# Performance work log

Hardware: AMD Instinct MI355X
Metric: run time of the kernel (lower is better)

The kernel has to match this reference:

```python
import jax, jax.numpy as jnp
import numpy as np

# (dy, dx) offsets corresponding to the single -1 entries of kernels 1..8
# delta1 rows: (0,0),(0,1),(0,2),(1,2); delta2 = spatial flip: (2,2),(2,1),(2,0),(1,0)
OFFSETS = [(-1, -1), (-1, 0), (-1, 1), (0, 1), (1, 1), (1, 0), (1, -1), (0, -1)]
NUM_LAYER = 9
EPS = 1e-12


def _shift(x, dy, dx):
    # zero-padded shift: out[y, x] = in[y + dy, x + dx]; dilation = shifts[0] = 1
    b, c, h, w = x.shape
    p = jnp.pad(x, ((0, 0), (0, 0), (1, 1), (1, 1)))
    return jax.lax.dynamic_slice(p, (0, 0, 1 + dy, 1 + dx), (b, c, h, w))


def _l2norm(v, axis):
    # matches torch.nn.functional.normalize: v / max(||v||, eps)
    n = jnp.sqrt(jnp.sum(v * v, axis=axis, keepdims=True))
    return v / jnp.maximum(n, EPS)


def setup_inputs() -> dict:
    key = jax.random.key(0)
    k1, k2, k3, k4 = jax.random.split(key, 4)
    B, C, H, W = 4, 256, 96, 96
    cen = jax.random.normal(k1, (B, C, H, W), dtype=jnp.float32)
    scale = 1.0 / np.sqrt(C)
    # grouped 1x1 convs (groups=9): per-group (C x C) weight matrices
    W1 = jax.random.normal(k2, (NUM_LAYER, C, C), dtype=jnp.float32) * scale
    W2 = jax.random.normal(k3, (C, C), dtype=jnp.float32) * scale
    W3 = jax.random.normal(k4, (NUM_LAYER, C, C), dtype=jnp.float32) * scale
    return {"cen": cen, "W1": W1, "W2": W2, "W3": W3}


def reference(cen, W1, W2, W3):
    b, c, h, w = cen.shape
    # Extract_layer: 8 fixed depthwise 3x3 convs (each = negated shift) + identity
    surrounds = jnp.stack(
        [-_shift(cen, dy, dx) for dy, dx in OFFSETS] + [cen], axis=1
    )  # (b, 9, c, h, w)
    # Analyze_layer: grouped 1x1 convs = per-group matmuls
    out1 = jnp.einsum("gij,bgjhw->bgihw", W1, surrounds)
    out2 = jnp.einsum("ij,bjhw->bihw", W2, cen)[:, None]  # (b, 1, c, h, w)
    out3 = jnp.einsum("gij,bgjhw->bgihw", W3, surrounds)
    out1 = _l2norm(out1, axis=2)
    out2 = _l2norm(out2, axis=2)
    out3 = _l2norm(out3, axis=2)
    # softmax over a size-1 axis (dim=2 after mean+keepdim) -> identically 1.0
    att = jax.nn.softmax(
        jnp.mean(out1 * out2, axis=2, keepdims=True), axis=2
    )  # (b, 9, 1, h, w)
    out = jnp.sum(att * out3, axis=1)  # (b, c, h, w)
    return out + cen
```

## Files before the change

kernel.cpp:

```cpp
#include <hip/hip_runtime.h>
#include <stdint.h>

#define BB 4
#define CC 256
#define HH 96
#define WW 96
#define HP 98
#define CP 264
#define XT 32
#define YT 4
#define XE 34

typedef __bf16 bf16x8 __attribute__((ext_vector_type(8)));
typedef __bf16 bf16x16 __attribute__((ext_vector_type(16)));
typedef float f32x4 __attribute__((ext_vector_type(4)));
typedef float f32x16 __attribute__((ext_vector_type(16)));

__device__ __forceinline__ uint16_t f2bf(float f) {
    uint32_t u = __float_as_uint(f);
    u += 0x7FFFu + ((u >> 16) & 1u);
    return (uint16_t)(u >> 16);
}

__global__ void zero_halo(uint16_t* __restrict__ cenT) {
    int idx = blockIdx.x * 256 + threadIdx.x;
    if (idx >= 1552 * 33) return;
    int p = idx / 33, q = idx - p * 33;
    int b = p / 388, s = p - b * 388;
    int y, x;
    if (s < 98)      { y = 0;       x = s; }
    else if (s < 196){ y = 97;      x = s - 98; }
    else if (s < 292){ x = 0;       y = s - 196 + 1; }
    else             { x = 97;      y = s - 292 + 1; }
    size_t o = (((size_t)b * HP + y) * HP + x) * CP + q * 8;
    *(uint4*)(cenT + o) = make_uint4(0u, 0u, 0u, 0u);
}

__global__ void transpose_cen(const float* __restrict__ cen, uint16_t* __restrict__ cenT) {
    const int y = blockIdx.x, b = blockIdx.y, ch = blockIdx.z, tid = threadIdx.x;
    __shared__ uint16_t ldsX[128 * 100];

    #pragma unroll
    for (int i = 0; i < 12; ++i) {
        int f = i * 256 + tid;
        int c = f / 24, xq = f % 24;
        float4 v = *(const float4*)(cen + ((((size_t)b * CC + ch * 128 + c) * HH + y) * WW + xq * 4));
        uint2 pk;
        pk.x = (uint32_t)f2bf(v.x) | ((uint32_t)f2bf(v.y) << 16);
        pk.y = (uint32_t)f2bf(v.z) | ((uint32_t)f2bf(v.w) << 16);
        *(uint2*)(&ldsX[c * 100 + xq * 4]) = pk;
    }
    __syncthreads();
    #pragma unroll
    for (int i = 0; i < 6; ++i) {
        int t = i * 256 + tid;
        int x = t % 96, cq = t / 96;
        uint32_t w0, w1, w2, w3;
        w0 = (uint32_t)ldsX[(cq * 8 + 0) * 100 + x] | ((uint32_t)ldsX[(cq * 8 + 1) * 100 + x] << 16);
        w1 = (uint32_t)ldsX[(cq * 8 + 2) * 100 + x] | ((uint32_t)ldsX[(cq * 8 + 3) * 100 + x] << 16);
        w2 = (uint32_t)ldsX[(cq * 8 + 4) * 100 + x] | ((uint32_t)ldsX[(cq * 8 + 5) * 100 + x] << 16);
        w3 = (uint32_t)ldsX[(cq * 8 + 6) * 100 + x] | ((uint32_t)ldsX[(cq * 8 + 7) * 100 + x] << 16);
        size_t o = (((size_t)b * HP + (y + 1)) * HP + (x + 1)) * CP + ch * 128 + cq * 8;
        *(uint4*)(cenT + o) = make_uint4(w0, w1, w2, w3);
    }
}

__global__ void cvt_w3(const float* __restrict__ W3, uint16_t* __restrict__ W3bf) {
    int e = (blockIdx.x * 256 + threadIdx.x) * 4;
    int g = e >> 16, n = (e >> 8) & 255, k = e & 255;
    float4 v = *(const float4*)(W3 + e);
    uint2 pk;
    pk.x = (uint32_t)f2bf(v.x) | ((uint32_t)f2bf(v.y) << 16);
    pk.y = (uint32_t)f2bf(v.z) | ((uint32_t)f2bf(v.w) << 16);
    size_t o = (size_t)(((g * 8 + (n >> 5)) * 16 + (k >> 4)) * 512)
             + (n & 31) * 16 + ((k >> 3) & 1) * 8 + (k & 7);
    *(uint2*)(W3bf + o) = pk;
}

__global__ __launch_bounds__(512, 2)
void ecm_main(const float* __restrict__ cen, const uint16_t* __restrict__ cenT,
              const uint16_t* __restrict__ W3bf, float* __restrict__ out) {
    const int tid = threadIdx.x;
    const int wv = tid >> 6, lane = tid & 63, col = lane & 31, kh = lane >> 5;
    const int c2 = wv & 3, p2 = wv >> 2;
    const int x0 = blockIdx.x * XT, y0 = blockIdx.y * YT, b = blockIdx.z;

    __shared__ __align__(16) uint16_t ldsA[6 * XE * CP];
    __shared__ __align__(16) float ldsP[2][128][4];

    const int dgOrd[9] = {0, 1, 2, 7, 8, 3, 6, 5, 4};

    for (int rr = 0; rr < 6; ++rr) {
        const uint4* gs = (const uint4*)(cenT + (((size_t)b * HP + (y0 + rr)) * HP + x0) * CP);
        uint4* ls = (uint4*)(ldsA + rr * XE * CP);
        for (int c = tid; c < XE * CP / 8; c += 512) ls[c] = gs[c];
    }
    __syncthreads();

    const uint16_t* wbA = W3bf + (size_t)(2 * c2) * (16 * 512) + col * 16 + kh * 8;
    bf16x16 finA0 = {}, finA1 = {}, finB0 = {}, finB1 = {};

    #pragma unroll 1
    for (int idx = 0; idx < 9; ++idx) {
        const int g = dgOrd[idx], dg = idx / 3, dx = idx % 3 - 1;

        const uint16_t* wgA = wbA + (size_t)g * 65536;
        const uint16_t* wgB = wgA + 16 * 512;
        const int a0 = ((dg + 2 * p2) * XE + (col + dx + 1)) * CP + kh * 8;
        const int a1 = a0 + XE * CP;

        f32x16 aA0 = {}, aA1 = {}, aB0 = {}, aB1 = {};

        bf16x8 qA[3], qB[3];
        #pragma unroll
        for (int i = 0; i < 3; ++i) {
            qA[i] = *(const bf16x8*)(wgA + i * 512);
            qB[i] = *(const bf16x8*)(wgB + i * 512);
        }
        bf16x8 b0 = *(const bf16x8*)(ldsA + a0);
        bf16x8 b1 = *(const bf16x8*)(ldsA + a1);

        #pragma unroll
        for (int ks = 0; ks < 16; ++ks) {
            bf16x8 wa = qA[ks % 3], wb = qB[ks % 3];
            if (ks + 3 < 16) {
                qA[ks % 3] = *(const bf16x8*)(wgA + (ks + 3) * 512);
                qB[ks % 3] = *(const bf16x8*)(wgB + (ks + 3) * 512);
            }
            bf16x8 n0 = b0, n1 = b1;
            if (ks + 1 < 16) {
                n0 = *(const bf16x8*)(ldsA + a0 + (ks + 1) * 16);
                n1 = *(const bf16x8*)(ldsA + a1 + (ks + 1) * 16);
            }
            __builtin_amdgcn_s_setprio(1);
            aA0 = __builtin_amdgcn_mfma_f32_32x32x16_bf16(wa, b0, aA0, 0, 0, 0);
            aB0 = __builtin_amdgcn_mfma_f32_32x32x16_bf16(wb, b0, aB0, 0, 0, 0);
            aA1 = __builtin_amdgcn_mfma_f32_32x32x16_bf16(wa, b1, aA1, 0, 0, 0);
            aB1 = __builtin_amdgcn_mfma_f32_32x32x16_bf16(wb, b1, aB1, 0, 0, 0);
            __builtin_amdgcn_s_setprio(0);
            b0 = n0; b1 = n1;
        }

        float s0 = 0.f, s1 = 0.f;
        #pragma unroll
        for (int r = 0; r < 16; ++r) {
            s0 += aA0[r] * aA0[r] + aB0[r] * aB0[r];
            s1 += aA1[r] * aA1[r] + aB1[r] * aB1[r];
        }
        s0 += __shfl_xor(s0, 32, 64);
        s1 += __shfl_xor(s1, 32, 64);
        if (kh == 0) {
            ldsP[idx & 1][(2 * p2) * 32 + col][c2] = s0;
            ldsP[idx & 1][(2 * p2 + 1) * 32 + col][c2] = s1;
        }
        __syncthreads();

        f32x4 pa = *(const f32x4*)&ldsP[idx & 1][(2 * p2) * 32 + col][0];
        f32x4 qa = *(const f32x4*)&ldsP[idx & 1][(2 * p2 + 1) * 32 + col][0];
        float n0 = pa[0] + pa[1] + pa[2] + pa[3];
        float n1 = qa[0] + qa[1] + qa[2] + qa[3];
        const float sgn = (g == 8) ? 1.f : -1.f;
        float sc0 = sgn / fmaxf(sqrtf(n0), 1e-12f);
        float sc1 = sgn / fmaxf(sqrtf(n1), 1e-12f);
        #pragma unroll
        for (int r = 0; r < 16; ++r) {
            finA0[r] = (__bf16)((float)finA0[r] + aA0[r] * sc0);
            finB0[r] = (__bf16)((float)finB0[r] + aB0[r] * sc0);
            finA1[r] = (__bf16)((float)finA1[r] + aA1[r] * sc1);
            finB1[r] = (__bf16)((float)finB1[r] + aB1[r] * sc1);
        }
    }

    #pragma unroll
    for (int r = 0; r < 16; ++r) {
        int chA = c2 * 64 + (r & 3) + 8 * (r >> 2) + 4 * kh;
        size_t oA0 = (((size_t)b * CC + chA) * HH + (y0 + 2 * p2)) * WW + (x0 + col);
        size_t oA1 = oA0 + WW;
        out[oA0] = (float)finA0[r] + cen[oA0];
        out[oA1] = (float)finA1[r] + cen[oA1];
        size_t oB0 = oA0 + (size_t)32 * HH * WW;
        size_t oB1 = oB0 + WW;
        out[oB0] = (float)finB0[r] + cen[oB0];
        out[oB1] = (float)finB1[r] + cen[oB1];
    }
}

extern "C" void kernel_launch(void* const* d_in, const int* in_sizes, int n_in,
                              void* d_out, int out_size, void* d_ws, size_t ws_size,
                              hipStream_t stream) {
    const float* cen = (const float*)d_in[0];
    const float* W3 = (const float*)d_in[3];
    float* out = (float*)d_out;

    uint16_t* cenT = (uint16_t*)d_ws;
    const size_t cenT_elems = (size_t)BB * HP * HP * CP;
    uint16_t* W3bf = cenT + cenT_elems;

    zero_halo<<<201, 256, 0, stream>>>(cenT);
    transpose_cen<<<dim3(HH, BB, 2), 256, 0, stream>>>(cen, cenT);
    cvt_w3<<<576, 256, 0, stream>>>(W3, W3bf);
    ecm_main<<<dim3(3, 24, 4), 512, 0, stream>>>(cen, cenT, W3bf, out);
}
```

Measured before the change: 185.6 us.

## Enlarge spatial tile to six rows so each wave computes three rows

Raises the tile height from 4 to 6 rows so each wave accumulates three output rows per weight fragment instead of two. This reuses each loaded W3 fragment across more MFMAs and lowers the relative halo load. In exchange it uses much more LDS, more accumulator registers and fewer blocks, and weight prefetch depth drops from three to two. That can reduce occupancy and leave compute units idle.

```diff
diff --git a/kernel.cpp b/kernel.cpp
--- a/kernel.cpp
+++ b/kernel.cpp
@@ -8,7 +8,7 @@
 #define HP 98
 #define CP 264
 #define XT 32
-#define YT 4
+#define YT 6
 #define XE 34
 
 typedef __bf16 bf16x8 __attribute__((ext_vector_type(8)));
@@ -82,15 +82,15 @@
               const uint16_t* __restrict__ W3bf, float* __restrict__ out) {
     const int tid = threadIdx.x;
     const int wv = tid >> 6, lane = tid & 63, col = lane & 31, kh = lane >> 5;
-    const int c2 = wv & 3, p2 = wv >> 2;
+    const int c2 = wv & 3, p3 = wv >> 2;
     const int x0 = blockIdx.x * XT, y0 = blockIdx.y * YT, b = blockIdx.z;
 
-    __shared__ __align__(16) uint16_t ldsA[6 * XE * CP];
-    __shared__ __align__(16) float ldsP[2][128][4];
+    __shared__ __align__(16) uint16_t ldsA[8 * XE * CP];
+    __shared__ __align__(16) float ldsP[2][192][4];
 
     const int dgOrd[9] = {0, 1, 2, 7, 8, 3, 6, 5, 4};
 
-    for (int rr = 0; rr < 6; ++rr) {
+    for (int rr = 0; rr < 8; ++rr) {
         const uint4* gs = (const uint4*)(cenT + (((size_t)b * HP + (y0 + rr)) * HP + x0) * CP);
         uint4* ls = (uint4*)(ldsA + rr * XE * CP);
         for (int c = tid; c < XE * CP / 8; c += 512) ls[c] = gs[c];
@@ -98,7 +98,7 @@
     __syncthreads();
 
     const uint16_t* wbA = W3bf + (size_t)(2 * c2) * (16 * 512) + col * 16 + kh * 8;
-    bf16x16 finA0 = {}, finA1 = {}, finB0 = {}, finB1 = {};
+    bf16x16 fA[3] = {}, fB[3] = {};
 
     #pragma unroll 1
     for (int idx = 0; idx < 9; ++idx) {
@@ -106,82 +106,85 @@
 
         const uint16_t* wgA = wbA + (size_t)g * 65536;
         const uint16_t* wgB = wgA + 16 * 512;
-        const int a0 = ((dg + 2 * p2) * XE + (col + dx + 1)) * CP + kh * 8;
-        const int a1 = a0 + XE * CP;
-
-        f32x16 aA0 = {}, aA1 = {}, aB0 = {}, aB1 = {};
-
-        bf16x8 qA[3], qB[3];
-        #pragma unroll
-        for (int i = 0; i < 3; ++i) {
-            qA[i] = *(const bf16x8*)(wgA + i * 512);
-            qB[i] = *(const bf16x8*)(wgB + i * 512);
-        }
-        bf16x8 b0 = *(const bf16x8*)(ldsA + a0);
-        bf16x8 b1 = *(const bf16x8*)(ldsA + a1);
+        int a[3];
+        #pragma unroll
+        for (int rr = 0; rr < 3; ++rr)
+            a[rr] = ((dg + 3 * p3 + rr) * XE + (col + dx + 1)) * CP + kh * 8;
+
+        f32x16 aA[3] = {}, aB[3] = {};
+
+        bf16x8 qA[2], qB[2];
+        qA[0] = *(const bf16x8*)(wgA);
+        qB[0] = *(const bf16x8*)(wgB);
+        qA[1] = *(const bf16x8*)(wgA + 512);
+        qB[1] = *(const bf16x8*)(wgB + 512);
+        bf16x8 bR[3];
+        #pragma unroll
+        for (int rr = 0; rr < 3; ++rr) bR[rr] = *(const bf16x8*)(ldsA + a[rr]);
 
         #pragma unroll
         for (int ks = 0; ks < 16; ++ks) {
-            bf16x8 wa = qA[ks % 3], wb = qB[ks % 3];
-            if (ks + 3 < 16) {
-                qA[ks % 3] = *(const bf16x8*)(wgA + (ks + 3) * 512);
-                qB[ks % 3] = *(const bf16x8*)(wgB + (ks + 3) * 512);
+            bf16x8 wa = qA[ks & 1], wb = qB[ks & 1];
+            if (ks + 2 < 16) {
+                qA[ks & 1] = *(const bf16x8*)(wgA + (ks + 2) * 512);
+                qB[ks & 1] = *(const bf16x8*)(wgB + (ks + 2) * 512);
             }
-            bf16x8 n0 = b0, n1 = b1;
-            if (ks + 1 < 16) {
-                n0 = *(const bf16x8*)(ldsA + a0 + (ks + 1) * 16);
-                n1 = *(const bf16x8*)(ldsA + a1 + (ks + 1) * 16);
+            bf16x8 bN[3];
+            #pragma unroll
+            for (int rr = 0; rr < 3; ++rr)
+                bN[rr] = (ks + 1 < 16) ? *(const bf16x8*)(ldsA + a[rr] + (ks + 1) * 16)
+                                       : bR[rr];
+            __builtin_amdgcn_s_setprio(1);
+            #pragma unroll
+            for (int rr = 0; rr < 3; ++rr) {
+                aA[rr] = __builtin_amdgcn_mfma_f32_32x32x16_bf16(wa, bR[rr], aA[rr], 0, 0, 0);
+                aB[rr] = __builtin_amdgcn_mfma_f32_32x32x16_bf16(wb, bR[rr], aB[rr], 0, 0, 0);
             }
-            __builtin_amdgcn_s_setprio(1);
-            aA0 = __builtin_amdgcn_mfma_f32_32x32x16_bf16(wa, b0, aA0, 0, 0, 0);
-            aB0 = __builtin_amdgcn_mfma_f32_32x32x16_bf16(wb, b0, aB0, 0, 0, 0);
-            aA1 = __builtin_amdgcn_mfma_f32_32x32x16_bf16(wa, b1, aA1, 0, 0, 0);
-            aB1 = __builtin_amdgcn_mfma_f32_32x32x16_bf16(wb, b1, aB1, 0, 0, 0);
             __builtin_amdgcn_s_setprio(0);
-            b0 = n0; b1 = n1;
-        }
-
-        float s0 = 0.f, s1 = 0.f;
+            #pragma unroll
+            for (int rr = 0; rr < 3; ++rr) bR[rr] = bN[rr];
+        }
+
+        float s[3];
+        #pragma unroll
+        for (int rr = 0; rr < 3; ++rr) {
+            float t = 0.f;
+            #pragma unroll
+            for (int r = 0; r < 16; ++r) t += aA[rr][r] * aA[rr][r] + aB[rr][r] * aB[rr][r];
+            t += __shfl_xor(t, 32, 64);
+            s[rr] = t;
+        }
+        if (kh == 0) {
+            #pragma unroll
+            for (int rr = 0; rr < 3; ++rr)
+                ldsP[idx & 1][(3 * p3 + rr) * 32 + col][c2] = s[rr];
+        }
+        __syncthreads();
+
+        const float sgn = (g == 8) ? 1.f : -1.f;
+        #pragma unroll
+        for (int rr = 0; rr < 3; ++rr) {
+            f32x4 pa = *(const f32x4*)&ldsP[idx & 1][(3 * p3 + rr) * 32 + col][0];
+            float n = pa[0] + pa[1] + pa[2] + pa[3];
+            float sc = sgn / fmaxf(sqrtf(n), 1e-12f);
+            #pragma unroll
+            for (int r = 0; r < 16; ++r) {
+                fA[rr][r] = (__bf16)((float)fA[rr][r] + aA[rr][r] * sc);
+                fB[rr][r] = (__bf16)((float)fB[rr][r] + aB[rr][r] * sc);
+            }
+        }
+    }
+
+    #pragma unroll
+    for (int rr = 0; rr < 3; ++rr) {
         #pragma unroll
         for (int r = 0; r < 16; ++r) {
-            s0 += aA0[r] * aA0[r] + aB0[r] * aB0[r];
-            s1 += aA1[r] * aA1[r] + aB1[r] * aB1[r];
-        }
-        s0 += __shfl_xor(s0, 32, 64);
-        s1 += __shfl_xor(s1, 32, 64);
-        if (kh == 0) {
-            ldsP[idx & 1][(2 * p2) * 32 + col][c2] = s0;
-            ldsP[idx & 1][(2 * p2 + 1) * 32 + col][c2] = s1;
-        }
-        __syncthreads();
-
-        f32x4 pa = *(const f32x4*)&ldsP[idx & 1][(2 * p2) * 32 + col][0];
-        f32x4 qa = *(const f32x4*)&ldsP[idx & 1][(2 * p2 + 1) * 32 + col][0];
-        float n0 = pa[0] + pa[1] + pa[2] + pa[3];
-        float n1 = qa[0] + qa[1] + qa[2] + qa[3];
-        const float sgn = (g == 8) ? 1.f : -1.f;
-        float sc0 = sgn / fmaxf(sqrtf(n0), 1e-12f);
-        float sc1 = sgn / fmaxf(sqrtf(n1), 1e-12f);
-        #pragma unroll
-        for (int r = 0; r < 16; ++r) {
-            finA0[r] = (__bf16)((float)finA0[r] + aA0[r] * sc0);
-            finB0[r] = (__bf16)((float)finB0[r] + aB0[r] * sc0);
-            finA1[r] = (__bf16)((float)finA1[r] + aA1[r] * sc1);
-            finB1[r] = (__bf16)((float)finB1[r] + aB1[r] * sc1);
-        }
-    }
-
-    #pragma unroll
-    for (int r = 0; r < 16; ++r) {
-        int chA = c2 * 64 + (r & 3) + 8 * (r >> 2) + 4 * kh;
-        size_t oA0 = (((size_t)b * CC + chA) * HH + (y0 + 2 * p2)) * WW + (x0 + col);
-        size_t oA1 = oA0 + WW;
-        out[oA0] = (float)finA0[r] + cen[oA0];
-        out[oA1] = (float)finA1[r] + cen[oA1];
-        size_t oB0 = oA0 + (size_t)32 * HH * WW;
-        size_t oB1 = oB0 + WW;
-        out[oB0] = (float)finB0[r] + cen[oB0];
-        out[oB1] = (float)finB1[r] + cen[oB1];
+            int chA = c2 * 64 + (r & 3) + 8 * (r >> 2) + 4 * kh;
+            size_t oA = (((size_t)b * CC + chA) * HH + (y0 + 3 * p3 + rr)) * WW + (x0 + col);
+            out[oA] = (float)fA[rr][r] + cen[oA];
+            size_t oB = oA + (size_t)32 * HH * WW;
+            out[oB] = (float)fB[rr][r] + cen[oB];
+        }
     }
 }
 
@@ -199,5 +202,5 @@
     zero_halo<<<201, 256, 0, stream>>>(cenT);
     transpose_cen<<<dim3(HH, BB, 2), 256, 0, stream>>>(cen, cenT);
     cvt_w3<<<576, 256, 0, stream>>>(W3, W3bf);
-    ecm_main<<<dim3(3, 24, 4), 512, 0, stream>>>(cen, cenT, W3bf, out);
-}
+    ecm_main<<<dim3(3, 16, 4), 512, 0, stream>>>(cen, cenT, W3bf, out);
+}
```

Result: faster. 160.8 us (-13.3%).
